# Kernel tuning notes

Measured on AMD Instinct MI355X. Metric: run time of the kernel, lower is better.

The kernel has to match this reference:

```python
import jax, jax.numpy as jnp
import numpy as np

NT, NJ = 100000, 300000
FT = FJ = 32
H, OUT = 64, 16
E_TJ = E_JT = 1000000
E_JJ = 2000000
# NormalParamExtractor default: biased_softplus(1.0) -> softplus(x + inv_softplus(1.0))
SP_BIAS = float(np.log(np.expm1(1.0)))


def setup_inputs() -> dict:
    key = jax.random.key(0)
    ks = jax.random.split(key, 64)
    ki = iter(range(64))
    def nrm(shape, fan_in):
        return jax.random.normal(ks[next(ki)], shape, jnp.float32) / np.sqrt(fan_in)
    d = {}
    d['x_torso'] = jax.random.normal(ks[next(ki)], (NT, FT), jnp.float32)
    d['x_joint'] = jax.random.normal(ks[next(ki)], (NJ, FJ), jnp.float32)
    def edges(e, n_src, n_dst):
        src = jax.random.randint(ks[next(ki)], (e,), 0, n_src, jnp.int32)
        dst = jax.random.randint(ks[next(ki)], (e,), 0, n_dst, jnp.int32)
        return jnp.stack([src, dst])
    d['ei_tj'] = edges(E_TJ, NT, NJ)
    d['ei_jt'] = edges(E_JT, NJ, NT)
    d['ei_jj'] = edges(E_JJ, NJ, NJ)
    d['w0_t'] = nrm((FT, H), FT); d['b0_t'] = jnp.zeros((H,), jnp.float32)
    d['w0_j'] = nrm((FJ, H), FJ); d['b0_j'] = jnp.zeros((H,), jnp.float32)
    for layer in ('c1', 'c2'):
        for et in ('tj', 'jt', 'jj'):
            d[f'{layer}_{et}_rel_w'] = nrm((H, H), H)
            d[f'{layer}_{et}_rel_b'] = jnp.zeros((H,), jnp.float32)
            d[f'{layer}_{et}_root_w'] = nrm((H, H), H)
    d['w3_t'] = nrm((H, OUT), H); d['b3_t'] = jnp.zeros((OUT,), jnp.float32)
    d['w3_j'] = nrm((H, OUT), H); d['b3_j'] = jnp.zeros((OUT,), jnp.float32)
    return d


def _graph_conv(x_src, x_dst, ei, rel_w, rel_b, root_w, n_dst):
    # PyG GraphConv: lin_rel(sum_{j in N(i)} x_j) + lin_root(x_i)
    msg = jax.ops.segment_sum(x_src[ei[0]], ei[1], num_segments=n_dst)
    return msg @ rel_w + rel_b + x_dst @ root_w


def reference(x_torso, x_joint, ei_tj, ei_jt, ei_jj,
              w0_t, b0_t, w0_j, b0_j,
              c1_tj_rel_w, c1_tj_rel_b, c1_tj_root_w,
              c1_jt_rel_w, c1_jt_rel_b, c1_jt_root_w,
              c1_jj_rel_w, c1_jj_rel_b, c1_jj_root_w,
              c2_tj_rel_w, c2_tj_rel_b, c2_tj_root_w,
              c2_jt_rel_w, c2_jt_rel_b, c2_jt_root_w,
              c2_jj_rel_w, c2_jj_rel_b, c2_jj_root_w,
              w3_t, b3_t, w3_j, b3_j):
    # per-node-type input Linear
    h_t = x_torso @ w0_t + b0_t  # [NT, 64]
    h_j = x_joint @ w0_j + b0_j  # [NJ, 64]
    # hetero GraphConv layer 1 (to_hetero sums per-edge-type outputs on dst)
    t1 = _graph_conv(h_j, h_t, ei_jt, c1_jt_rel_w, c1_jt_rel_b, c1_jt_root_w, NT)
    j1 = (_graph_conv(h_t, h_j, ei_tj, c1_tj_rel_w, c1_tj_rel_b, c1_tj_root_w, NJ)
          + _graph_conv(h_j, h_j, ei_jj, c1_jj_rel_w, c1_jj_rel_b, c1_jj_root_w, NJ))
    h_t, h_j = jnp.tanh(t1), jnp.tanh(j1)
    # layer 2
    t2 = _graph_conv(h_j, h_t, ei_jt, c2_jt_rel_w, c2_jt_rel_b, c2_jt_root_w, NT)
    j2 = (_graph_conv(h_t, h_j, ei_tj, c2_tj_rel_w, c2_tj_rel_b, c2_tj_root_w, NJ)
          + _graph_conv(h_j, h_j, ei_jj, c2_jj_rel_w, c2_jj_rel_b, c2_jj_root_w, NJ))
    h_t, h_j = jnp.tanh(t2), jnp.tanh(j2)
    # output Linear + tanh per node type
    o_t = jnp.tanh(h_t @ w3_t + b3_t)  # [NT, 16]
    o_j = jnp.tanh(h_j @ w3_j + b3_j)  # [NJ, 16]
    # NormalParamExtractor: chunk last dim, biased softplus on scale
    loc_t, s_t = jnp.split(o_t, 2, axis=-1)
    loc_j, s_j = jnp.split(o_j, 2, axis=-1)
    scale_t = jax.nn.softplus(s_t + SP_BIAS)
    scale_j = jax.nn.softplus(s_j + SP_BIAS)
    return (loc_t, scale_t, loc_j, scale_j)
```

## Files before the change

kernel.cpp:

```cpp
#include <hip/hip_runtime.h>
#include <math.h>

constexpr int NT = 100000;
constexpr int NJ = 300000;
constexpr int E_TJ = 1000000, E_JT = 1000000, E_JJ = 2000000;
constexpr float SP_BIAS = 0.5413248546129181f;

__global__ void k_zero(int* __restrict__ p, int n) {
    int i = blockIdx.x * 256 + threadIdx.x;
    if (i < n) p[i] = 0;
}

__global__ void k_prep(const float* __restrict__ wa, const float* __restrict__ wb,
                       const float* __restrict__ ba, const float* __restrict__ bb,
                       float* __restrict__ wcomb, float* __restrict__ bcomb) {
    int i = blockIdx.x * 256 + threadIdx.x;
    if (i < 4096) wcomb[i] = wa[i] + wb[i];
    else if (i < 4160) bcomb[i - 4096] = ba[i - 4096] + bb[i - 4096];
}

__global__ void k_count(const int* __restrict__ dst, int E, int* __restrict__ deg) {
    int e = blockIdx.x * blockDim.x + threadIdx.x;
    if (e < E) atomicAdd(&deg[dst[e]], 1);
}

__global__ __launch_bounds__(1024) void k_bsum(const int* __restrict__ deg, int n,
                                               int* __restrict__ bsum) {
    __shared__ int s[1024];
    int i = blockIdx.x * 1024 + threadIdx.x;
    s[threadIdx.x] = (i < n) ? deg[i] : 0;
    __syncthreads();
    for (int d = 512; d > 0; d >>= 1) {
        if (threadIdx.x < d) s[threadIdx.x] += s[threadIdx.x + d];
        __syncthreads();
    }
    if (threadIdx.x == 0) bsum[blockIdx.x] = s[0];
}

__global__ __launch_bounds__(1024) void k_scan_bsum(int* bsum, int nb) {
    __shared__ int s[1024];
    int t = threadIdx.x;
    int v = (t < nb) ? bsum[t] : 0;
    s[t] = v;
    __syncthreads();
    for (int d = 1; d < 1024; d <<= 1) {
        int x = (t >= d) ? s[t - d] : 0;
        __syncthreads();
        s[t] += x;
        __syncthreads();
    }
    if (t < nb) bsum[t] = s[t] - v;
}

__global__ __launch_bounds__(1024) void k_scan_final(const int* __restrict__ deg, int n,
                                                     const int* __restrict__ bsum,
                                                     int* __restrict__ off,
                                                     int* __restrict__ cur) {
    __shared__ int s[1024];
    int t = threadIdx.x;
    int i = blockIdx.x * 1024 + t;
    int v = (i < n) ? deg[i] : 0;
    s[t] = v;
    __syncthreads();
    for (int d = 1; d < 1024; d <<= 1) {
        int x = (t >= d) ? s[t - d] : 0;
        __syncthreads();
        s[t] += x;
        __syncthreads();
    }
    int incl = s[t];
    int base = bsum[blockIdx.x];
    if (i < n) {
        int excl = base + incl - v;
        off[i] = excl;
        cur[i] = excl;
        if (i == n - 1) off[n] = base + incl;
    }
}

__global__ void k_fill(const int* __restrict__ src, const int* __restrict__ dst, int E,
                       int* __restrict__ cur, int* __restrict__ out_src, int src_ofs) {
    int e = blockIdx.x * blockDim.x + threadIdx.x;
    if (e < E) {
        int p = atomicAdd(&cur[dst[e]], 1);
        out_src[p] = (src[e] + src_ofs) * 64;
    }
}

__global__ __launch_bounds__(256) void k_in_linear(const float* __restrict__ x,
        const float* __restrict__ w, const float* __restrict__ b,
        float* __restrict__ h, int n) {
    __shared__ float ws_[32 * 64];
    __shared__ __align__(16) float xs_[512];
    for (int i = threadIdx.x; i < 32 * 64; i += 256) ws_[i] = w[i];
    __syncthreads();
    const int wslot = (threadIdx.x >> 6) & 3;
    const int lane = threadIdx.x & 63;
    const int lo = lane & 31;
    float* xsw = &xs_[wslot * 128];
    int wave = (blockIdx.x * 256 + threadIdx.x) >> 6;
    int nq = (n + 3) >> 2;
    int nwaves = gridDim.x * 4;
    float bv = b[lane];
    for (int q = wave; q < nq; q += nwaves) {
        int i0 = q * 4;
        int i1 = i0 + 1 < n ? i0 + 1 : n - 1;
        int i2 = i0 + 2 < n ? i0 + 2 : n - 1;
        int i3 = i0 + 3 < n ? i0 + 3 : n - 1;
        xsw[lane]      = (lane < 32) ? x[(size_t)i0 * 32 + lo] : x[(size_t)i1 * 32 + lo];
        xsw[64 + lane] = (lane < 32) ? x[(size_t)i2 * 32 + lo] : x[(size_t)i3 * 32 + lo];
        float r0 = bv, r1 = bv, r2 = bv, r3 = bv;
        const float4* xq = (const float4*)xsw;
        #pragma unroll
        for (int c = 0; c < 8; ++c) {
            float4 x0 = xq[c], x1 = xq[8 + c], x2 = xq[16 + c], x3 = xq[24 + c];
            float wA = ws_[(4 * c + 0) * 64 + lane];
            float wB = ws_[(4 * c + 1) * 64 + lane];
            float wC = ws_[(4 * c + 2) * 64 + lane];
            float wD = ws_[(4 * c + 3) * 64 + lane];
            r0 += x0.x * wA + x0.y * wB + x0.z * wC + x0.w * wD;
            r1 += x1.x * wA + x1.y * wB + x1.z * wC + x1.w * wD;
            r2 += x2.x * wA + x2.y * wB + x2.z * wC + x2.w * wD;
            r3 += x3.x * wA + x3.y * wB + x3.z * wC + x3.w * wD;
        }
        h[(size_t)i0 * 64 + lane] = r0;
        if (i0 + 1 < n) h[(size_t)i1 * 64 + lane] = r1;
        if (i0 + 2 < n) h[(size_t)i2 * 64 + lane] = r2;
        if (i0 + 3 < n) h[(size_t)i3 * 64 + lane] = r3;
    }
}

__global__ __launch_bounds__(256, 4) void k_transform(const float* __restrict__ h,
        const float* __restrict__ w, float* __restrict__ a, int n) {
    __shared__ float ws_[64 * 64];
    __shared__ __align__(16) float hs_[1024];
    for (int i = threadIdx.x; i < 64 * 64; i += 256) ws_[i] = w[i];
    __syncthreads();
    const int wslot = (threadIdx.x >> 6) & 3;
    const int lane = threadIdx.x & 63;
    float* hsw = &hs_[wslot * 256];
    int wave = (blockIdx.x * 256 + threadIdx.x) >> 6;
    int nq = (n + 3) >> 2;
    int nwaves = gridDim.x * 4;
    for (int q = wave; q < nq; q += nwaves) {
        int i0 = q * 4;
        int i1 = i0 + 1 < n ? i0 + 1 : n - 1;
        int i2 = i0 + 2 < n ? i0 + 2 : n - 1;
        int i3 = i0 + 3 < n ? i0 + 3 : n - 1;
        hsw[lane]       = h[(size_t)i0 * 64 + lane];
        hsw[64 + lane]  = h[(size_t)i1 * 64 + lane];
        hsw[128 + lane] = h[(size_t)i2 * 64 + lane];
        hsw[192 + lane] = h[(size_t)i3 * 64 + lane];
        float r0 = 0.f, r1 = 0.f, r2 = 0.f, r3 = 0.f;
        const float4* hq = (const float4*)hsw;
        #pragma unroll 4
        for (int c = 0; c < 16; ++c) {
            float4 h0 = hq[c], h1 = hq[16 + c], h2 = hq[32 + c], h3 = hq[48 + c];
            float wA = ws_[(4 * c + 0) * 64 + lane];
            float wB = ws_[(4 * c + 1) * 64 + lane];
            float wC = ws_[(4 * c + 2) * 64 + lane];
            float wD = ws_[(4 * c + 3) * 64 + lane];
            r0 += h0.x * wA + h0.y * wB + h0.z * wC + h0.w * wD;
            r1 += h1.x * wA + h1.y * wB + h1.z * wC + h1.w * wD;
            r2 += h2.x * wA + h2.y * wB + h2.z * wC + h2.w * wD;
            r3 += h3.x * wA + h3.y * wB + h3.z * wC + h3.w * wD;
        }
        a[(size_t)i0 * 64 + lane] = r0;
        if (i0 + 1 < n) a[(size_t)i1 * 64 + lane] = r1;
        if (i0 + 2 < n) a[(size_t)i2 * 64 + lane] = r2;
        if (i0 + 3 < n) a[(size_t)i3 * 64 + lane] = r3;
    }
}

__global__ __launch_bounds__(256, 4) void k_transform2(float* __restrict__ h,
        const float* __restrict__ wa, const float* __restrict__ wb,
        const float* __restrict__ bias, float* __restrict__ outa, int n) {
    __shared__ float wsa_[64 * 64];
    __shared__ float wsb_[64 * 64];
    __shared__ __align__(16) float hs_[1024];
    for (int i = threadIdx.x; i < 64 * 64; i += 256) { wsa_[i] = wa[i]; wsb_[i] = wb[i]; }
    __syncthreads();
    const int wslot = (threadIdx.x >> 6) & 3;
    const int lane = threadIdx.x & 63;
    float* hsw = &hs_[wslot * 256];
    int wave = (blockIdx.x * 256 + threadIdx.x) >> 6;
    int nq = (n + 3) >> 2;
    int nwaves = gridDim.x * 4;
    float bv = bias[lane];
    for (int q = wave; q < nq; q += nwaves) {
        int i0 = q * 4;
        int i1 = i0 + 1 < n ? i0 + 1 : n - 1;
        int i2 = i0 + 2 < n ? i0 + 2 : n - 1;
        int i3 = i0 + 3 < n ? i0 + 3 : n - 1;
        hsw[lane]       = h[(size_t)i0 * 64 + lane];
        hsw[64 + lane]  = h[(size_t)i1 * 64 + lane];
        hsw[128 + lane] = h[(size_t)i2 * 64 + lane];
        hsw[192 + lane] = h[(size_t)i3 * 64 + lane];
        float ra0 = 0.f, ra1 = 0.f, ra2 = 0.f, ra3 = 0.f;
        float rb0 = bv, rb1 = bv, rb2 = bv, rb3 = bv;
        const float4* hq = (const float4*)hsw;
        #pragma unroll 4
        for (int c = 0; c < 16; ++c) {
            float4 h0 = hq[c], h1 = hq[16 + c], h2 = hq[32 + c], h3 = hq[48 + c];
            float aA = wsa_[(4 * c + 0) * 64 + lane];
            float aB = wsa_[(4 * c + 1) * 64 + lane];
            float aC = wsa_[(4 * c + 2) * 64 + lane];
            float aD = wsa_[(4 * c + 3) * 64 + lane];
            ra0 += h0.x * aA + h0.y * aB + h0.z * aC + h0.w * aD;
            ra1 += h1.x * aA + h1.y * aB + h1.z * aC + h1.w * aD;
            ra2 += h2.x * aA + h2.y * aB + h2.z * aC + h2.w * aD;
            ra3 += h3.x * aA + h3.y * aB + h3.z * aC + h3.w * aD;
            float bA = wsb_[(4 * c + 0) * 64 + lane];
            float bB = wsb_[(4 * c + 1) * 64 + lane];
            float bC = wsb_[(4 * c + 2) * 64 + lane];
            float bD = wsb_[(4 * c + 3) * 64 + lane];
            rb0 += h0.x * bA + h0.y * bB + h0.z * bC + h0.w * bD;
            rb1 += h1.x * bA + h1.y * bB + h1.z * bC + h1.w * bD;
            rb2 += h2.x * bA + h2.y * bB + h2.z * bC + h2.w * bD;
            rb3 += h3.x * bA + h3.y * bB + h3.z * bC + h3.w * bD;
        }
        outa[(size_t)i0 * 64 + lane] = ra0;
        h[(size_t)i0 * 64 + lane] = rb0;
        if (i0 + 1 < n) { outa[(size_t)i1 * 64 + lane] = ra1; h[(size_t)i1 * 64 + lane] = rb1; }
        if (i0 + 2 < n) { outa[(size_t)i2 * 64 + lane] = ra2; h[(size_t)i2 * 64 + lane] = rb2; }
        if (i0 + 3 < n) { outa[(size_t)i3 * 64 + lane] = ra3; h[(size_t)i3 * 64 + lane] = rb3; }
    }
}

__global__ __launch_bounds__(256) void k_aggadd(const float* __restrict__ a,
        float* __restrict__ h,
        const int* __restrict__ off, const int* __restrict__ srcs, int n) {
    int wave = (blockIdx.x * 256 + threadIdx.x) >> 6;
    int lane = threadIdx.x & 63;
    int nwaves = gridDim.x * 4;
    for (int i = wave; i < n; i += nwaves) {
        int e0 = off[i], e1 = off[i + 1];
        float acc = h[(size_t)i * 64 + lane];
        for (int base = e0; base < e1; base += 64) {
            int rem = e1 - base;
            int cnt = rem < 64 ? rem : 64;
            int idx = (lane < cnt) ? srcs[base + lane] : 0;
            int k = 0;
            for (; k + 8 <= cnt; k += 8) {
                int s0 = __shfl(idx, k),     s1 = __shfl(idx, k + 1);
                int s2 = __shfl(idx, k + 2), s3 = __shfl(idx, k + 3);
                int s4 = __shfl(idx, k + 4), s5 = __shfl(idx, k + 5);
                int s6 = __shfl(idx, k + 6), s7 = __shfl(idx, k + 7);
                float v0 = a[(size_t)s0 + lane], v1 = a[(size_t)s1 + lane];
                float v2 = a[(size_t)s2 + lane], v3 = a[(size_t)s3 + lane];
                float v4 = a[(size_t)s4 + lane], v5 = a[(size_t)s5 + lane];
                float v6 = a[(size_t)s6 + lane], v7 = a[(size_t)s7 + lane];
                acc += ((v0 + v1) + (v2 + v3)) + ((v4 + v5) + (v6 + v7));
            }
            for (; k < cnt; ++k)
                acc += a[(size_t)__shfl(idx, k) + lane];
        }
        h[(size_t)i * 64 + lane] = tanhf(acc);
    }
}

__global__ __launch_bounds__(256) void k_out(const float* __restrict__ h,
        const float* __restrict__ w3, const float* __restrict__ b3,
        float* __restrict__ loc, float* __restrict__ scale, int n) {
    __shared__ float ws_[64 * 16];
    __shared__ __align__(16) float hs_[1024];
    for (int i = threadIdx.x; i < 64 * 16; i += 256) ws_[i] = w3[i];
    __syncthreads();
    const int wslot = (threadIdx.x >> 6) & 3;
    const int lane = threadIdx.x & 63;
    const int m = lane >> 4;
    const int o = lane & 15;
    float* hsw = &hs_[wslot * 256];
    int wave = (blockIdx.x * 256 + threadIdx.x) >> 6;
    int nq = (n + 3) >> 2;
    int nwaves = gridDim.x * 4;
    float bv = b3[o];
    for (int q = wave; q < nq; q += nwaves) {
        int i0 = q * 4;
        int i1 = i0 + 1 < n ? i0 + 1 : n - 1;
        int i2 = i0 + 2 < n ? i0 + 2 : n - 1;
        int i3 = i0 + 3 < n ? i0 + 3 : n - 1;
        hsw[lane]       = h[(size_t)i0 * 64 + lane];
        hsw[64 + lane]  = h[(size_t)i1 * 64 + lane];
        hsw[128 + lane] = h[(size_t)i2 * 64 + lane];
        hsw[192 + lane] = h[(size_t)i3 * 64 + lane];
        float acc = bv;
        const float4* hq = (const float4*)&hsw[m * 64];
        #pragma unroll
        for (int c = 0; c < 16; ++c) {
            float4 hv = hq[c];
            acc += hv.x * ws_[(4 * c + 0) * 16 + o];
            acc += hv.y * ws_[(4 * c + 1) * 16 + o];
            acc += hv.z * ws_[(4 * c + 2) * 16 + o];
            acc += hv.w * ws_[(4 * c + 3) * 16 + o];
        }
        int im = (m == 0) ? i0 : (m == 1) ? i1 : (m == 2) ? i2 : i3;
        bool valid = (i0 + m < n) || (m == 0);
        float v = tanhf(acc);
        if (valid) {
            if (o < 8) {
                loc[(size_t)im * 8 + o] = v;
            } else {
                float xx = v + SP_BIAS;
                float sp = (xx > 20.f) ? xx : log1pf(expf(xx));
                scale[(size_t)im * 8 + (o - 8)] = sp;
            }
        }
    }
}

extern "C" void kernel_launch(void* const* d_in, const int* in_sizes, int n_in,
                              void* d_out, int out_size, void* d_ws, size_t ws_size,
                              hipStream_t stream) {
    const float* x_t  = (const float*)d_in[0];
    const float* x_j  = (const float*)d_in[1];
    const int*   ei_tj = (const int*)d_in[2];
    const int*   ei_jt = (const int*)d_in[3];
    const int*   ei_jj = (const int*)d_in[4];
    const float* w0_t = (const float*)d_in[5];
    const float* b0_t = (const float*)d_in[6];
    const float* w0_j = (const float*)d_in[7];
    const float* b0_j = (const float*)d_in[8];
    const float* w3_t = (const float*)d_in[27];
    const float* b3_t = (const float*)d_in[28];
    const float* w3_j = (const float*)d_in[29];
    const float* b3_j = (const float*)d_in[30];

    float* fws   = (float*)d_ws;
    float* Q     = fws;
    float* P     = Q + (size_t)NT * 64;
    float* h_t   = P + (size_t)NJ * 64;
    float* h_j   = h_t + (size_t)NT * 64;
    float* wcomb = h_j + (size_t)NJ * 64;
    float* bcomb = wcomb + 64 * 64;
    int* iws    = (int*)(bcomb + 64);
    int* off_jt = iws;
    int* cur_jt = off_jt + NT + 1;
    int* off_cj = cur_jt + NT;
    int* cur_cj = off_cj + NJ + 1;
    int* src_jt = cur_cj + NJ;
    int* src_cj = src_jt + E_JT;
    int* bsum   = src_cj + E_TJ + E_JJ;

    size_t required = ((char*)(bsum + 1024)) - ((char*)d_ws);
    if (ws_size < required) return;

    int zcount = 2 * NT + 2 * NJ + 2;
    k_zero<<<(zcount + 255) / 256, 256, 0, stream>>>(iws, zcount);
    k_count<<<(E_JT + 255) / 256, 256, 0, stream>>>(ei_jt + E_JT, E_JT, cur_jt);
    k_count<<<(E_TJ + 255) / 256, 256, 0, stream>>>(ei_tj + E_TJ, E_TJ, cur_cj);
    k_count<<<(E_JJ + 255) / 256, 256, 0, stream>>>(ei_jj + E_JJ, E_JJ, cur_cj);

    auto scan = [&](int* cur, int* off, int n) {
        int nb = (n + 1023) / 1024;
        k_bsum<<<nb, 1024, 0, stream>>>(cur, n, bsum);
        k_scan_bsum<<<1, 1024, 0, stream>>>(bsum, nb);
        k_scan_final<<<nb, 1024, 0, stream>>>(cur, n, bsum, off, cur);
    };
    scan(cur_jt, off_jt, NT);
    scan(cur_cj, off_cj, NJ);

    k_fill<<<(E_JT + 255) / 256, 256, 0, stream>>>(ei_jt, ei_jt + E_JT, E_JT, cur_jt, src_jt, 0);
    k_fill<<<(E_TJ + 255) / 256, 256, 0, stream>>>(ei_tj, ei_tj + E_TJ, E_TJ, cur_cj, src_cj, 0);
    k_fill<<<(E_JJ + 255) / 256, 256, 0, stream>>>(ei_jj, ei_jj + E_JJ, E_JJ, cur_cj, src_cj, NT);

    k_in_linear<<<2048, 256, 0, stream>>>(x_t, w0_t, b0_t, h_t, NT);
    k_in_linear<<<2048, 256, 0, stream>>>(x_j, w0_j, b0_j, h_j, NJ);

    for (int l = 0; l < 2; ++l) {
        const float* tj_rel_w  = (const float*)d_in[9 + l * 9 + 0];
        const float* tj_rel_b  = (const float*)d_in[9 + l * 9 + 1];
        const float* tj_root_w = (const float*)d_in[9 + l * 9 + 2];
        const float* jt_rel_w  = (const float*)d_in[9 + l * 9 + 3];
        const float* jt_rel_b  = (const float*)d_in[9 + l * 9 + 4];
        const float* jt_root_w = (const float*)d_in[9 + l * 9 + 5];
        const float* jj_rel_w  = (const float*)d_in[9 + l * 9 + 6];
        const float* jj_rel_b  = (const float*)d_in[9 + l * 9 + 7];
        const float* jj_root_w = (const float*)d_in[9 + l * 9 + 8];

        k_prep<<<17, 256, 0, stream>>>(tj_root_w, jj_root_w, tj_rel_b, jj_rel_b, wcomb, bcomb);

        k_transform2<<<2048, 256, 0, stream>>>(h_t, tj_rel_w, jt_root_w, jt_rel_b, Q, NT);
        k_transform<<<2048, 256, 0, stream>>>(h_j, jt_rel_w, P, NJ);
        k_aggadd<<<2048, 256, 0, stream>>>(P, h_t, off_jt, src_jt, NT);
        k_transform2<<<2048, 256, 0, stream>>>(h_j, jj_rel_w, wcomb, bcomb, P, NJ);
        k_aggadd<<<2048, 256, 0, stream>>>(Q, h_j, off_cj, src_cj, NJ);
    }

    float* out = (float*)d_out;
    k_out<<<2048, 256, 0, stream>>>(h_t, w3_t, b3_t,
                                    out, out + (size_t)NT * 8, NT);
    k_out<<<2048, 256, 0, stream>>>(h_j, w3_j, b3_j,
                                    out + (size_t)2 * NT * 8,
                                    out + (size_t)2 * NT * 8 + (size_t)NJ * 8, NJ);
}
```

Before: 1.397 ms.

## Batch edge counting/filling per thread and merge per-type linear launches

The count and fill kernels now handle eight edges per thread with a grid-stride layout, issuing the index loads before the atomics to raise memory-level parallelism. The two input-linear launches and the two output launches are each merged into one launch that splits blocks between torso and joint nodes, saving launches and tail effects. The launch-bounds occupancy hint on k_transform is raised from 4 to 6 waves. Grouping eight atomics per thread adds register pressure, and the fixed 512/1536 block split may not balance torso and joint work exactly.

```diff
diff --git a/kernel.cpp b/kernel.cpp
--- a/kernel.cpp
+++ b/kernel.cpp
@@ -20,8 +20,17 @@
 }
 
 __global__ void k_count(const int* __restrict__ dst, int E, int* __restrict__ deg) {
-    int e = blockIdx.x * blockDim.x + threadIdx.x;
-    if (e < E) atomicAdd(&deg[dst[e]], 1);
+    int t = blockIdx.x * blockDim.x + threadIdx.x;
+    int S = gridDim.x * blockDim.x;
+    int e[8]; int d[8];
+    #pragma unroll
+    for (int r = 0; r < 8; ++r) {
+        e[r] = t + r * S;
+        d[r] = (e[r] < E) ? dst[e[r]] : 0;
+    }
+    #pragma unroll
+    for (int r = 0; r < 8; ++r)
+        if (e[r] < E) atomicAdd(&deg[d[r]], 1);
 }
 
 __global__ __launch_bounds__(1024) void k_bsum(const int* __restrict__ deg, int n,
@@ -80,16 +89,26 @@
 
 __global__ void k_fill(const int* __restrict__ src, const int* __restrict__ dst, int E,
                        int* __restrict__ cur, int* __restrict__ out_src, int src_ofs) {
-    int e = blockIdx.x * blockDim.x + threadIdx.x;
-    if (e < E) {
-        int p = atomicAdd(&cur[dst[e]], 1);
-        out_src[p] = (src[e] + src_ofs) * 64;
-    }
-}
-
-__global__ __launch_bounds__(256) void k_in_linear(const float* __restrict__ x,
+    int t = blockIdx.x * blockDim.x + threadIdx.x;
+    int S = gridDim.x * blockDim.x;
+    int e[8]; int d[8]; int s[8]; int p[8];
+    #pragma unroll
+    for (int r = 0; r < 8; ++r) {
+        e[r] = t + r * S;
+        d[r] = (e[r] < E) ? dst[e[r]] : 0;
+        s[r] = (e[r] < E) ? src[e[r]] : 0;
+    }
+    #pragma unroll
+    for (int r = 0; r < 8; ++r)
+        p[r] = (e[r] < E) ? atomicAdd(&cur[d[r]], 1) : 0;
+    #pragma unroll
+    for (int r = 0; r < 8; ++r)
+        if (e[r] < E) out_src[p[r]] = (s[r] + src_ofs) * 64;
+}
+
+__device__ __forceinline__ void inlin_body(const float* __restrict__ x,
         const float* __restrict__ w, const float* __restrict__ b,
-        float* __restrict__ h, int n) {
+        float* __restrict__ h, int n, int blk_local, int nblk) {
     __shared__ float ws_[32 * 64];
     __shared__ __align__(16) float xs_[512];
     for (int i = threadIdx.x; i < 32 * 64; i += 256) ws_[i] = w[i];
@@ -98,9 +117,9 @@
     const int lane = threadIdx.x & 63;
     const int lo = lane & 31;
     float* xsw = &xs_[wslot * 128];
-    int wave = (blockIdx.x * 256 + threadIdx.x) >> 6;
+    int wave = (blk_local * 256 + (int)threadIdx.x) >> 6;
     int nq = (n + 3) >> 2;
-    int nwaves = gridDim.x * 4;
+    int nwaves = nblk * 4;
     float bv = b[lane];
     for (int q = wave; q < nq; q += nwaves) {
         int i0 = q * 4;
@@ -130,7 +149,16 @@
     }
 }
 
-__global__ __launch_bounds__(256, 4) void k_transform(const float* __restrict__ h,
+__global__ __launch_bounds__(256) void k_in_linear2(const float* __restrict__ x_t,
+        const float* __restrict__ w_t, const float* __restrict__ b_t, float* __restrict__ h_t,
+        const float* __restrict__ x_j, const float* __restrict__ w_j,
+        const float* __restrict__ b_j, float* __restrict__ h_j, int bt) {
+    int blk = blockIdx.x;
+    if (blk < bt) inlin_body(x_t, w_t, b_t, h_t, NT, blk, bt);
+    else          inlin_body(x_j, w_j, b_j, h_j, NJ, blk - bt, (int)gridDim.x - bt);
+}
+
+__global__ __launch_bounds__(256, 6) void k_transform(const float* __restrict__ h,
         const float* __restrict__ w, float* __restrict__ a, int n) {
     __shared__ float ws_[64 * 64];
     __shared__ __align__(16) float hs_[1024];
@@ -259,9 +287,10 @@
     }
 }
 
-__global__ __launch_bounds__(256) void k_out(const float* __restrict__ h,
+__device__ __forceinline__ void out_body(const float* __restrict__ h,
         const float* __restrict__ w3, const float* __restrict__ b3,
-        float* __restrict__ loc, float* __restrict__ scale, int n) {
+        float* __restrict__ loc, float* __restrict__ scale, int n,
+        int blk_local, int nblk) {
     __shared__ float ws_[64 * 16];
     __shared__ __align__(16) float hs_[1024];
     for (int i = threadIdx.x; i < 64 * 16; i += 256) ws_[i] = w3[i];
@@ -271,9 +300,9 @@
     const int m = lane >> 4;
     const int o = lane & 15;
     float* hsw = &hs_[wslot * 256];
-    int wave = (blockIdx.x * 256 + threadIdx.x) >> 6;
+    int wave = (blk_local * 256 + (int)threadIdx.x) >> 6;
     int nq = (n + 3) >> 2;
-    int nwaves = gridDim.x * 4;
+    int nwaves = nblk * 4;
     float bv = b3[o];
     for (int q = wave; q < nq; q += nwaves) {
         int i0 = q * 4;
@@ -309,6 +338,17 @@
     }
 }
 
+__global__ __launch_bounds__(256) void k_out2(const float* __restrict__ h_t,
+        const float* __restrict__ w3_t, const float* __restrict__ b3_t,
+        float* __restrict__ loc_t, float* __restrict__ scale_t,
+        const float* __restrict__ h_j, const float* __restrict__ w3_j,
+        const float* __restrict__ b3_j,
+        float* __restrict__ loc_j, float* __restrict__ scale_j, int bt) {
+    int blk = blockIdx.x;
+    if (blk < bt) out_body(h_t, w3_t, b3_t, loc_t, scale_t, NT, blk, bt);
+    else          out_body(h_j, w3_j, b3_j, loc_j, scale_j, NJ, blk - bt, (int)gridDim.x - bt);
+}
+
 extern "C" void kernel_launch(void* const* d_in, const int* in_sizes, int n_in,
                               void* d_out, int out_size, void* d_ws, size_t ws_size,
                               hipStream_t stream) {
@@ -347,9 +387,9 @@
 
     int zcount = 2 * NT + 2 * NJ + 2;
     k_zero<<<(zcount + 255) / 256, 256, 0, stream>>>(iws, zcount);
-    k_count<<<(E_JT + 255) / 256, 256, 0, stream>>>(ei_jt + E_JT, E_JT, cur_jt);
-    k_count<<<(E_TJ + 255) / 256, 256, 0, stream>>>(ei_tj + E_TJ, E_TJ, cur_cj);
-    k_count<<<(E_JJ + 255) / 256, 256, 0, stream>>>(ei_jj + E_JJ, E_JJ, cur_cj);
+    k_count<<<(E_JT / 8 + 255) / 256, 256, 0, stream>>>(ei_jt + E_JT, E_JT, cur_jt);
+    k_count<<<(E_TJ / 8 + 255) / 256, 256, 0, stream>>>(ei_tj + E_TJ, E_TJ, cur_cj);
+    k_count<<<(E_JJ / 8 + 255) / 256, 256, 0, stream>>>(ei_jj + E_JJ, E_JJ, cur_cj);
 
     auto scan = [&](int* cur, int* off, int n) {
         int nb = (n + 1023) / 1024;
@@ -360,12 +400,12 @@
     scan(cur_jt, off_jt, NT);
     scan(cur_cj, off_cj, NJ);
 
-    k_fill<<<(E_JT + 255) / 256, 256, 0, stream>>>(ei_jt, ei_jt + E_JT, E_JT, cur_jt, src_jt, 0);
-    k_fill<<<(E_TJ + 255) / 256, 256, 0, stream>>>(ei_tj, ei_tj + E_TJ, E_TJ, cur_cj, src_cj, 0);
-    k_fill<<<(E_JJ + 255) / 256, 256, 0, stream>>>(ei_jj, ei_jj + E_JJ, E_JJ, cur_cj, src_cj, NT);
-
-    k_in_linear<<<2048, 256, 0, stream>>>(x_t, w0_t, b0_t, h_t, NT);
-    k_in_linear<<<2048, 256, 0, stream>>>(x_j, w0_j, b0_j, h_j, NJ);
+    k_fill<<<(E_JT / 8 + 255) / 256, 256, 0, stream>>>(ei_jt, ei_jt + E_JT, E_JT, cur_jt, src_jt, 0);
+    k_fill<<<(E_TJ / 8 + 255) / 256, 256, 0, stream>>>(ei_tj, ei_tj + E_TJ, E_TJ, cur_cj, src_cj, 0);
+    k_fill<<<(E_JJ / 8 + 255) / 256, 256, 0, stream>>>(ei_jj, ei_jj + E_JJ, E_JJ, cur_cj, src_cj, NT);
+
+    k_in_linear2<<<2048, 256, 0, stream>>>(x_t, w0_t, b0_t, h_t,
+                                           x_j, w0_j, b0_j, h_j, 512);
 
     for (int l = 0; l < 2; ++l) {
         const float* tj_rel_w  = (const float*)d_in[9 + l * 9 + 0];
@@ -388,9 +428,9 @@
     }
 
     float* out = (float*)d_out;
-    k_out<<<2048, 256, 0, stream>>>(h_t, w3_t, b3_t,
-                                    out, out + (size_t)NT * 8, NT);
-    k_out<<<2048, 256, 0, stream>>>(h_j, w3_j, b3_j,
-                                    out + (size_t)2 * NT * 8,
-                                    out + (size_t)2 * NT * 8 + (size_t)NJ * 8, NJ);
-}
+    k_out2<<<2048, 256, 0, stream>>>(h_t, w3_t, b3_t,
+                                     out, out + (size_t)NT * 8,
+                                     h_j, w3_j, b3_j,
+                                     out + (size_t)2 * NT * 8,
+                                     out + (size_t)2 * NT * 8 + (size_t)NJ * 8, 512);
+}
```

Measured after the change: 1.339 ms. 4.2% less time.
